# Optimization experiments

Hardware: AMD Instinct MI355X
Metric: run time of the kernel (lower is better)

Reference implementation:

```python
import jax, jax.numpy as jnp
import numpy as np

R = 2  # radius from sigma_wh == 1: int((1*6 - 1)/2) = 2 -> fixed 5x5 patch
P = 2 * R + 1

# Design matrix for log-domain Gaussian least-squares fit:
# log z = c0 + c1*x + c2*y + c3*x^2 + c4*y^2
_ys, _xs = np.meshgrid(np.arange(-R, R + 1), np.arange(-R, R + 1), indexing='ij')
_xs = _xs.reshape(-1).astype(np.float32)
_ys = _ys.reshape(-1).astype(np.float32)
_M = np.stack([np.ones_like(_xs), _xs, _ys, _xs ** 2, _ys ** 2], axis=1)  # [25,5]
PINV = jnp.asarray(np.linalg.pinv(_M))  # [5,25]


def _neg_loss(pred, gt):
    pos = (gt == 1.0).astype(pred.dtype)
    neg = (gt < 1.0).astype(pred.dtype)
    neg_w = (1.0 - gt) ** 4
    pos_loss = (jnp.log(pred) * (1.0 - pred) ** 2 * pos).sum()
    neg_loss = (jnp.log(1.0 - pred) * pred ** 2 * neg_w * neg).sum()
    num_pos = pos.sum()
    denom = jnp.where(num_pos == 0, 1.0, num_pos)
    return jnp.where(num_pos == 0, -neg_loss, -(pos_loss + neg_loss) / denom)


def setup_inputs() -> dict:
    key = jax.random.key(0)
    k1, k2, k3, k4 = jax.random.split(key, 4)
    B, C, H, W, O = 8, 80, 128, 128, 128
    return {
        'hm_out': jax.random.normal(k1, (B, C, H, W), jnp.float32),
        'hm_gt': jax.random.uniform(k2, (B, C, H, W), jnp.float32),
        'ct_ind': jax.random.randint(k3, (B, C, O, 2), 0, 124).astype(jnp.int32),
        'sigma_wh': jnp.ones((B, C, O, 2), jnp.float32),
        'hm_mask': jnp.ones((B, C, H, W), jnp.float32),
        'sigmawh_mask': jax.random.randint(k4, (B, C, O), 0, 2).astype(jnp.int32),
    }


def reference(hm_out, hm_gt, ct_ind, sigma_wh, hm_mask, sigmawh_mask):
    B, C, H, W = hm_out.shape
    O = ct_ind.shape[2]

    # --- focal loss (second call in original overwrites the first) ---
    hm_s = jax.nn.sigmoid(hm_out)
    pred = jnp.clip(hm_s, 1e-6, 1.0 - 1e-6)
    focal = _neg_loss(pred, hm_gt * hm_mask)

    # --- batched per-object 5x5 patch gather (replaces python triple loop) ---
    x = jnp.clip(ct_ind[..., 0], R, W - 1 - R)  # [B,C,O]
    y = jnp.clip(ct_ind[..., 1], R, H - 1 - R)
    off = jnp.arange(-R, R + 1)
    yy = y[..., None, None] + off[:, None]            # [B,C,O,P,1]
    xx = x[..., None, None] + off[None, :]            # [B,C,O,1,P]
    b_idx = jnp.arange(B)[:, None, None, None, None]
    c_idx = jnp.arange(C)[None, :, None, None, None]
    patch = hm_s[b_idx, c_idx, yy, xx]                # [B,C,O,P,P]
    logz = jnp.log(patch).reshape(B, C, O, P * P)

    # --- batched gaussian fit: least squares in log domain ---
    coef = jnp.einsum('bcop,kp->bcok', logz, PINV)    # [B,C,O,5]
    bx, by, ax, ay = coef[..., 1], coef[..., 2], coef[..., 3], coef[..., 4]
    ax_s = jnp.where(jnp.abs(ax) < 1e-12, -1.0, ax)
    ay_s = jnp.where(jnp.abs(ay) < 1e-12, -1.0, ay)
    sw2 = -0.5 / ax_s   # fitted variance along w
    sh2 = -0.5 / ay_s   # fitted variance along h
    mu_w = -bx / (2.0 * ax_s)
    mu_h = -by / (2.0 * ay_s)

    # original loop: obj in range(mask.sum()) and mask[obj]==1
    cnt = sigmawh_mask.sum(axis=-1)                                  # [B,C]
    in_loop = jnp.arange(O)[None, None, :] < cnt[..., None]
    valid = (sigmawh_mask == 1) & in_loop & (sw2 > 0) & (sh2 > 0)

    sgw = sigma_wh[..., 0]
    sgh = sigma_wh[..., 1]
    osw = jnp.where(valid, sw2, 1.0)
    osh = jnp.where(valid, sh2, 1.0)
    omw = jnp.where(valid, mu_w, 0.0)
    omh = jnp.where(valid, mu_h, 0.0)
    sgw2 = jnp.where(valid, sgw, 1.0) ** 2
    sgh2 = jnp.where(valid, sgh, 1.0) ** 2

    kl = (0.5 * jnp.log(sgw2 * sgh2 / (osw * osh)) - 1.0
          + 0.5 * (osw / sgw2 + osh / sgh2)
          + 0.5 * (omw ** 2 / sgw2 + omh ** 2 / sgh2))
    kl_sum = jnp.where(valid, kl, 0.0).sum()
    return (kl_sum, focal)
```

## Files before the change

### kernel.cpp

```cpp
#include <hip/hip_runtime.h>
#include <math.h>

#define Bn 8
#define Cn 80
#define Hn 128
#define Wn 128
#define On 128

#define FOCAL_BLOCKS 2560
#define FOCAL_THREADS 256
#define FOCAL_ITERS 4

#define WS_PL 0
#define WS_NL 2560
#define WS_NP 5120
#define WS_KL 7680
#define KL_BLOCKS (Bn * Cn)

#define LOG_EPS -13.815511f
#define LOG_1MEPS -1.0000005e-6f

__global__ __launch_bounds__(FOCAL_THREADS) void focal_kernel(
    const float4* __restrict__ hm_out, const float4* __restrict__ hm_gt,
    const float4* __restrict__ hm_mask, double* __restrict__ ws) {
    const int base = blockIdx.x * (FOCAL_THREADS * FOCAL_ITERS) + threadIdx.x;

    float4 xo[FOCAL_ITERS], xg[FOCAL_ITERS], xm[FOCAL_ITERS];
#pragma unroll
    for (int it = 0; it < FOCAL_ITERS; ++it) {
        int i = base + it * FOCAL_THREADS;
        xo[it] = hm_out[i];
        xg[it] = hm_gt[i];
        xm[it] = hm_mask[i];
    }

    float pl = 0.0f, nl = 0.0f, npos = 0.0f;
#pragma unroll
    for (int it = 0; it < FOCAL_ITERS; ++it) {
        const float* po = (const float*)&xo[it];
        const float* pg = (const float*)&xg[it];
        const float* pm = (const float*)&xm[it];
#pragma unroll
        for (int k = 0; k < 4; ++k) {
            float x = po[k];
            float g = pg[k] * pm[k];
            float e = expf(-x);
            float s = 1.0f / (1.0f + e);
            float ls = -logf(1.0f + e);
            float l1s = ls - x;
            float ls_c = fminf(fmaxf(ls, LOG_EPS), LOG_1MEPS);
            float l1s_c = fminf(fmaxf(l1s, LOG_EPS), LOG_1MEPS);
            float pred = fminf(fmaxf(s, 1e-6f), 1.0f - 1e-6f);

            float om = 1.0f - pred;
            float pos_c = ls_c * om * om;
            float omg = 1.0f - g;
            float w4 = omg * omg;
            w4 *= w4;
            float neg_c = l1s_c * pred * pred * w4;

            bool is_pos = (g == 1.0f);
            bool is_neg = (g < 1.0f);
            pl += is_pos ? pos_c : 0.0f;
            npos += is_pos ? 1.0f : 0.0f;
            nl += is_neg ? neg_c : 0.0f;
        }
    }

    for (int off = 32; off > 0; off >>= 1) {
        pl += __shfl_down(pl, off, 64);
        nl += __shfl_down(nl, off, 64);
        npos += __shfl_down(npos, off, 64);
    }
    __shared__ double sm[3 * (FOCAL_THREADS / 64)];
    int wave = threadIdx.x >> 6;
    int lane = threadIdx.x & 63;
    if (lane == 0) {
        sm[wave * 3 + 0] = (double)pl;
        sm[wave * 3 + 1] = (double)nl;
        sm[wave * 3 + 2] = (double)npos;
    }
    __syncthreads();
    if (threadIdx.x == 0) {
        double a = 0, b = 0, c = 0;
#pragma unroll
        for (int w = 0; w < FOCAL_THREADS / 64; ++w) {
            a += sm[w * 3 + 0];
            b += sm[w * 3 + 1];
            c += sm[w * 3 + 2];
        }
        ws[WS_PL + blockIdx.x] = a;
        ws[WS_NL + blockIdx.x] = b;
        ws[WS_NP + blockIdx.x] = c;
    }
}

__global__ __launch_bounds__(On) void kl_kernel(
    const float* __restrict__ hm_out, const int* __restrict__ ct_ind,
    const float* __restrict__ sigma_wh, const int* __restrict__ sigmawh_mask,
    double* __restrict__ ws) {
    int bc = blockIdx.x;
    int o = threadIdx.x;

    int m = sigmawh_mask[bc * On + o];

    __shared__ int smi[On];
    smi[o] = m;
    __syncthreads();
    for (int s = On / 2; s > 0; s >>= 1) {
        if (o < s) smi[o] += smi[o + s];
        __syncthreads();
    }
    int cnt = smi[0];

    float kl = 0.0f;
    if (m == 1 && o < cnt) {
        int xi = ct_ind[(bc * On + o) * 2 + 0];
        int yi = ct_ind[(bc * On + o) * 2 + 1];
        xi = min(max(xi, 2), Wn - 3);
        yi = min(max(yi, 2), Hn - 3);

        const float* base = hm_out + ((size_t)bc * Hn + yi) * Wn + xi;

        float v[25];
#pragma unroll
        for (int py = 0; py < 5; ++py)
#pragma unroll
            for (int px = 0; px < 5; ++px)
                v[py * 5 + px] = base[(py - 2) * Wn + (px - 2)];

        float Sbx = 0.f, Sby = 0.f, Sax = 0.f, Say = 0.f;
#pragma unroll
        for (int py = 0; py < 5; ++py) {
#pragma unroll
            for (int px = 0; px < 5; ++px) {
                float x = v[py * 5 + px];
                float lz = -logf(1.0f + expf(-x));
                float fx = (float)(px - 2), fy = (float)(py - 2);
                Sbx += fx * lz;
                Sby += fy * lz;
                Sax += (fx * fx - 2.0f) * lz;
                Say += (fy * fy - 2.0f) * lz;
            }
        }
        float bx = Sbx * (1.0f / 50.0f);
        float by = Sby * (1.0f / 50.0f);
        float ax = Sax * (1.0f / 70.0f);
        float ay = Say * (1.0f / 70.0f);

        float ax_s = (fabsf(ax) < 1e-12f) ? -1.0f : ax;
        float ay_s = (fabsf(ay) < 1e-12f) ? -1.0f : ay;
        float sw2 = -0.5f / ax_s;
        float sh2 = -0.5f / ay_s;

        if (sw2 > 0.0f && sh2 > 0.0f) {
            float mw = -bx / (2.0f * ax_s);
            float mh = -by / (2.0f * ay_s);
            float sgw = sigma_wh[(bc * On + o) * 2 + 0];
            float sgh = sigma_wh[(bc * On + o) * 2 + 1];
            float sgw2 = sgw * sgw;
            float sgh2 = sgh * sgh;
            kl = 0.5f * logf(sgw2 * sgh2 / (sw2 * sh2)) - 1.0f +
                 0.5f * (sw2 / sgw2 + sh2 / sgh2) +
                 0.5f * (mw * mw / sgw2 + mh * mh / sgh2);
        }
    }

    for (int off = 32; off > 0; off >>= 1) kl += __shfl_down(kl, off, 64);
    __shared__ double smd[On / 64];
    int wave = o >> 6;
    int lane = o & 63;
    if (lane == 0) smd[wave] = (double)kl;
    __syncthreads();
    if (o == 0) ws[WS_KL + bc] = smd[0] + smd[1];
}

__global__ __launch_bounds__(256) void finalize_kernel(
    const double* __restrict__ ws, float* __restrict__ out) {
    int t = threadIdx.x;
    double pl = 0, nl = 0, np = 0, kl = 0;
    for (int i = t; i < FOCAL_BLOCKS; i += 256) {
        pl += ws[WS_PL + i];
        nl += ws[WS_NL + i];
        np += ws[WS_NP + i];
    }
    for (int i = t; i < KL_BLOCKS; i += 256) kl += ws[WS_KL + i];

    __shared__ double sm[4 * 256];
    sm[t] = pl;
    sm[256 + t] = nl;
    sm[512 + t] = np;
    sm[768 + t] = kl;
    __syncthreads();
    for (int s = 128; s > 0; s >>= 1) {
        if (t < s) {
            sm[t] += sm[t + s];
            sm[256 + t] += sm[256 + t + s];
            sm[512 + t] += sm[512 + t + s];
            sm[768 + t] += sm[768 + t + s];
        }
        __syncthreads();
    }
    if (t == 0) {
        double focal = (sm[512] == 0.0) ? (-sm[256]) : (-(sm[0] + sm[256]) / sm[512]);
        out[0] = (float)sm[768];
        out[1] = (float)focal;
    }
}

extern "C" void kernel_launch(void* const* d_in, const int* in_sizes, int n_in,
                              void* d_out, int out_size, void* d_ws,
                              size_t ws_size, hipStream_t stream) {
    const float* hm_out       = (const float*)d_in[0];
    const float* hm_gt        = (const float*)d_in[1];
    const int*   ct_ind       = (const int*)d_in[2];
    const float* sigma_wh     = (const float*)d_in[3];
    const float* hm_mask      = (const float*)d_in[4];
    const int*   sigmawh_mask = (const int*)d_in[5];
    double* ws = (double*)d_ws;
    float* out = (float*)d_out;

    focal_kernel<<<FOCAL_BLOCKS, FOCAL_THREADS, 0, stream>>>(
        (const float4*)hm_out, (const float4*)hm_gt, (const float4*)hm_mask, ws);

    kl_kernel<<<KL_BLOCKS, On, 0, stream>>>(hm_out, ct_ind, sigma_wh,
                                            sigmawh_mask, ws);

    finalize_kernel<<<1, 256, 0, stream>>>(ws, out);
}
```

Baseline: 164.8 us.

## Fuse focal and KL kernels into one launch with lane-parallel patch fits

Merges the focal-loss and KL kernels into a single launch whose block ranges pick the role. The focal part now uses 2048 blocks with 5 float4 iterations each, and switches to fast __expf/__logf intrinsics. The KL part gives each object 32 lanes, one per pixel of its 5x5 patch, with shuffle reductions instead of one serial thread per object. The aim is to remove a launch boundary, let the KL work overlap the bandwidth-bound focal pass, and shorten the KL latency chain. The costs are slightly lower precision from the intrinsics and redundant mask-count reductions in every KL block.

```diff
diff --git a/kernel.cpp b/kernel.cpp
--- a/kernel.cpp
+++ b/kernel.cpp
@@ -7,203 +7,218 @@
 #define Wn 128
 #define On 128
 
-#define FOCAL_BLOCKS 2560
+#define FOCAL_BLOCKS 2048
 #define FOCAL_THREADS 256
-#define FOCAL_ITERS 4
+#define FOCAL_ITERS 5
+
+#define KL_BLOCKS (Bn * Cn * On / 8)
+#define TOTAL_BLOCKS (FOCAL_BLOCKS + KL_BLOCKS)
 
 #define WS_PL 0
-#define WS_NL 2560
-#define WS_NP 5120
-#define WS_KL 7680
-#define KL_BLOCKS (Bn * Cn)
+#define WS_NL FOCAL_BLOCKS
+#define WS_NP (2 * FOCAL_BLOCKS)
+#define WS_KL (3 * FOCAL_BLOCKS)
 
 #define LOG_EPS -13.815511f
 #define LOG_1MEPS -1.0000005e-6f
 
-__global__ __launch_bounds__(FOCAL_THREADS) void focal_kernel(
-    const float4* __restrict__ hm_out, const float4* __restrict__ hm_gt,
-    const float4* __restrict__ hm_mask, double* __restrict__ ws) {
-    const int base = blockIdx.x * (FOCAL_THREADS * FOCAL_ITERS) + threadIdx.x;
-
-    float4 xo[FOCAL_ITERS], xg[FOCAL_ITERS], xm[FOCAL_ITERS];
-#pragma unroll
-    for (int it = 0; it < FOCAL_ITERS; ++it) {
-        int i = base + it * FOCAL_THREADS;
-        xo[it] = hm_out[i];
-        xg[it] = hm_gt[i];
-        xm[it] = hm_mask[i];
-    }
-
-    float pl = 0.0f, nl = 0.0f, npos = 0.0f;
-#pragma unroll
-    for (int it = 0; it < FOCAL_ITERS; ++it) {
-        const float* po = (const float*)&xo[it];
-        const float* pg = (const float*)&xg[it];
-        const float* pm = (const float*)&xm[it];
-#pragma unroll
-        for (int k = 0; k < 4; ++k) {
-            float x = po[k];
-            float g = pg[k] * pm[k];
-            float e = expf(-x);
-            float s = 1.0f / (1.0f + e);
-            float ls = -logf(1.0f + e);
-            float l1s = ls - x;
-            float ls_c = fminf(fmaxf(ls, LOG_EPS), LOG_1MEPS);
-            float l1s_c = fminf(fmaxf(l1s, LOG_EPS), LOG_1MEPS);
-            float pred = fminf(fmaxf(s, 1e-6f), 1.0f - 1e-6f);
-
-            float om = 1.0f - pred;
-            float pos_c = ls_c * om * om;
-            float omg = 1.0f - g;
-            float w4 = omg * omg;
-            w4 *= w4;
-            float neg_c = l1s_c * pred * pred * w4;
-
-            bool is_pos = (g == 1.0f);
-            bool is_neg = (g < 1.0f);
-            pl += is_pos ? pos_c : 0.0f;
-            npos += is_pos ? 1.0f : 0.0f;
-            nl += is_neg ? neg_c : 0.0f;
-        }
-    }
+__global__ __launch_bounds__(256) void fused_kernel(
+    const float4* __restrict__ hm_out4, const float4* __restrict__ hm_gt4,
+    const float4* __restrict__ hm_mask4, const float* __restrict__ hm_out,
+    const int* __restrict__ ct_ind, const float* __restrict__ sigma_wh,
+    const int* __restrict__ sigmawh_mask, double* __restrict__ ws) {
+    __shared__ double sd[16];
+    __shared__ int si[128];
+
+    const int t = threadIdx.x;
+
+    if (blockIdx.x < FOCAL_BLOCKS) {
+        const int bid = blockIdx.x;
+        const int base = bid * (FOCAL_THREADS * FOCAL_ITERS) + t;
+
+        float4 xo[FOCAL_ITERS], xg[FOCAL_ITERS], xm[FOCAL_ITERS];
+#pragma unroll
+        for (int it = 0; it < FOCAL_ITERS; ++it)
+            xo[it] = hm_out4[base + it * FOCAL_THREADS];
+#pragma unroll
+        for (int it = 0; it < FOCAL_ITERS; ++it)
+            xg[it] = hm_gt4[base + it * FOCAL_THREADS];
+#pragma unroll
+        for (int it = 0; it < FOCAL_ITERS; ++it)
+            xm[it] = hm_mask4[base + it * FOCAL_THREADS];
+
+        float pl = 0.0f, nl = 0.0f, np = 0.0f;
+#pragma unroll
+        for (int it = 0; it < FOCAL_ITERS; ++it) {
+            const float* po = (const float*)&xo[it];
+            const float* pg = (const float*)&xg[it];
+            const float* pm = (const float*)&xm[it];
+#pragma unroll
+            for (int k = 0; k < 4; ++k) {
+                float x = po[k];
+                float g = pg[k] * pm[k];
+                float e = __expf(-x);
+                float s = 1.0f / (1.0f + e);
+                float ls = -__logf(1.0f + e);
+                float l1s = ls - x;
+                float ls_c = fminf(fmaxf(ls, LOG_EPS), LOG_1MEPS);
+                float l1s_c = fminf(fmaxf(l1s, LOG_EPS), LOG_1MEPS);
+                float pred = fminf(fmaxf(s, 1e-6f), 1.0f - 1e-6f);
+
+                float om = 1.0f - pred;
+                float pos_c = ls_c * om * om;
+                float omg = 1.0f - g;
+                float w4 = omg * omg;
+                w4 *= w4;
+                float neg_c = l1s_c * pred * pred * w4;
+
+                bool is_pos = (g == 1.0f);
+                bool is_neg = (g < 1.0f);
+                pl += is_pos ? pos_c : 0.0f;
+                np += is_pos ? 1.0f : 0.0f;
+                nl += is_neg ? neg_c : 0.0f;
+            }
+        }
+
+        for (int off = 32; off > 0; off >>= 1) {
+            pl += __shfl_down(pl, off, 64);
+            nl += __shfl_down(nl, off, 64);
+            np += __shfl_down(np, off, 64);
+        }
+        int wave = t >> 6, lane = t & 63;
+        if (lane == 0) {
+            sd[wave * 3 + 0] = (double)pl;
+            sd[wave * 3 + 1] = (double)nl;
+            sd[wave * 3 + 2] = (double)np;
+        }
+        __syncthreads();
+        if (t == 0) {
+            double a = 0, b = 0, c = 0;
+#pragma unroll
+            for (int w = 0; w < 4; ++w) {
+                a += sd[w * 3 + 0];
+                b += sd[w * 3 + 1];
+                c += sd[w * 3 + 2];
+            }
+            ws[WS_PL + bid] = a;
+            ws[WS_NL + bid] = b;
+            ws[WS_NP + bid] = c;
+        }
+    } else {
+        const int kb = blockIdx.x - FOCAL_BLOCKS;
+        const int bc = kb >> 4;
+        const int o_base = (kb & 15) * 8;
+
+        if (t < 128) si[t] = sigmawh_mask[bc * On + t];
+        __syncthreads();
+
+        const int w = t >> 6, lane = t & 63;
+        const int half = lane >> 5, pix = lane & 31;
+        const int o = o_base + w * 2 + half;
+        const int m = si[o];
+        __syncthreads();
+        for (int s = 64; s > 0; s >>= 1) {
+            if (t < s) si[t] += si[t + s];
+            __syncthreads();
+        }
+        const int cnt = si[0];
+
+        float kl = 0.0f;
+        if (m == 1 && o < cnt) {
+            int gi = (bc * On + o) * 2;
+            int xi = min(max(ct_ind[gi + 0], 2), Wn - 3);
+            int yi = min(max(ct_ind[gi + 1], 2), Hn - 3);
+
+            float Sbx = 0.f, Sby = 0.f, Sax = 0.f, Say = 0.f;
+            if (pix < 25) {
+                int py = pix / 5;
+                int px = pix - py * 5;
+                float v = hm_out[((size_t)bc * Hn + (yi + py - 2)) * Wn +
+                                 (xi + px - 2)];
+                float lz = -__logf(1.0f + __expf(-v));
+                float fx = (float)(px - 2), fy = (float)(py - 2);
+                Sbx = fx * lz;
+                Sby = fy * lz;
+                Sax = (fx * fx - 2.0f) * lz;
+                Say = (fy * fy - 2.0f) * lz;
+            }
+#pragma unroll
+            for (int off = 16; off > 0; off >>= 1) {
+                Sbx += __shfl_xor(Sbx, off, 64);
+                Sby += __shfl_xor(Sby, off, 64);
+                Sax += __shfl_xor(Sax, off, 64);
+                Say += __shfl_xor(Say, off, 64);
+            }
+            float bx = Sbx * (1.0f / 50.0f);
+            float by = Sby * (1.0f / 50.0f);
+            float ax = Sax * (1.0f / 70.0f);
+            float ay = Say * (1.0f / 70.0f);
+
+            float ax_s = (fabsf(ax) < 1e-12f) ? -1.0f : ax;
+            float ay_s = (fabsf(ay) < 1e-12f) ? -1.0f : ay;
+            float sw2 = -0.5f / ax_s;
+            float sh2 = -0.5f / ay_s;
+
+            if (sw2 > 0.0f && sh2 > 0.0f) {
+                float mw = -bx / (2.0f * ax_s);
+                float mh = -by / (2.0f * ay_s);
+                float sgw = sigma_wh[gi + 0];
+                float sgh = sigma_wh[gi + 1];
+                float sgw2 = sgw * sgw;
+                float sgh2 = sgh * sgh;
+                kl = 0.5f * __logf(sgw2 * sgh2 / (sw2 * sh2)) - 1.0f +
+                     0.5f * (sw2 / sgw2 + sh2 / sgh2) +
+                     0.5f * (mw * mw / sgw2 + mh * mh / sgh2);
+            }
+        }
+        if (pix == 0) sd[w * 2 + half] = (double)kl;
+        __syncthreads();
+        if (t == 0) {
+            double s = 0;
+#pragma unroll
+            for (int i = 0; i < 8; ++i) s += sd[i];
+            ws[WS_KL + kb] = s;
+        }
+    }
+}
+
+__global__ __launch_bounds__(1024) void finalize_kernel(
+    const double* __restrict__ ws, float* __restrict__ out) {
+    int t = threadIdx.x;
+    double pl = 0, nl = 0, np = 0, kl = 0;
+    for (int i = t; i < FOCAL_BLOCKS; i += 1024) {
+        pl += ws[WS_PL + i];
+        nl += ws[WS_NL + i];
+        np += ws[WS_NP + i];
+    }
+    for (int i = t; i < KL_BLOCKS; i += 1024) kl += ws[WS_KL + i];
 
     for (int off = 32; off > 0; off >>= 1) {
         pl += __shfl_down(pl, off, 64);
         nl += __shfl_down(nl, off, 64);
-        npos += __shfl_down(npos, off, 64);
-    }
-    __shared__ double sm[3 * (FOCAL_THREADS / 64)];
-    int wave = threadIdx.x >> 6;
-    int lane = threadIdx.x & 63;
+        np += __shfl_down(np, off, 64);
+        kl += __shfl_down(kl, off, 64);
+    }
+    __shared__ double sm[16 * 4];
+    int wave = t >> 6, lane = t & 63;
     if (lane == 0) {
-        sm[wave * 3 + 0] = (double)pl;
-        sm[wave * 3 + 1] = (double)nl;
-        sm[wave * 3 + 2] = (double)npos;
+        sm[wave * 4 + 0] = pl;
+        sm[wave * 4 + 1] = nl;
+        sm[wave * 4 + 2] = np;
+        sm[wave * 4 + 3] = kl;
     }
     __syncthreads();
-    if (threadIdx.x == 0) {
-        double a = 0, b = 0, c = 0;
-#pragma unroll
-        for (int w = 0; w < FOCAL_THREADS / 64; ++w) {
-            a += sm[w * 3 + 0];
-            b += sm[w * 3 + 1];
-            c += sm[w * 3 + 2];
-        }
-        ws[WS_PL + blockIdx.x] = a;
-        ws[WS_NL + blockIdx.x] = b;
-        ws[WS_NP + blockIdx.x] = c;
-    }
-}
-
-__global__ __launch_bounds__(On) void kl_kernel(
-    const float* __restrict__ hm_out, const int* __restrict__ ct_ind,
-    const float* __restrict__ sigma_wh, const int* __restrict__ sigmawh_mask,
-    double* __restrict__ ws) {
-    int bc = blockIdx.x;
-    int o = threadIdx.x;
-
-    int m = sigmawh_mask[bc * On + o];
-
-    __shared__ int smi[On];
-    smi[o] = m;
-    __syncthreads();
-    for (int s = On / 2; s > 0; s >>= 1) {
-        if (o < s) smi[o] += smi[o + s];
-        __syncthreads();
-    }
-    int cnt = smi[0];
-
-    float kl = 0.0f;
-    if (m == 1 && o < cnt) {
-        int xi = ct_ind[(bc * On + o) * 2 + 0];
-        int yi = ct_ind[(bc * On + o) * 2 + 1];
-        xi = min(max(xi, 2), Wn - 3);
-        yi = min(max(yi, 2), Hn - 3);
-
-        const float* base = hm_out + ((size_t)bc * Hn + yi) * Wn + xi;
-
-        float v[25];
-#pragma unroll
-        for (int py = 0; py < 5; ++py)
-#pragma unroll
-            for (int px = 0; px < 5; ++px)
-                v[py * 5 + px] = base[(py - 2) * Wn + (px - 2)];
-
-        float Sbx = 0.f, Sby = 0.f, Sax = 0.f, Say = 0.f;
-#pragma unroll
-        for (int py = 0; py < 5; ++py) {
-#pragma unroll
-            for (int px = 0; px < 5; ++px) {
-                float x = v[py * 5 + px];
-                float lz = -logf(1.0f + expf(-x));
-                float fx = (float)(px - 2), fy = (float)(py - 2);
-                Sbx += fx * lz;
-                Sby += fy * lz;
-                Sax += (fx * fx - 2.0f) * lz;
-                Say += (fy * fy - 2.0f) * lz;
-            }
-        }
-        float bx = Sbx * (1.0f / 50.0f);
-        float by = Sby * (1.0f / 50.0f);
-        float ax = Sax * (1.0f / 70.0f);
-        float ay = Say * (1.0f / 70.0f);
-
-        float ax_s = (fabsf(ax) < 1e-12f) ? -1.0f : ax;
-        float ay_s = (fabsf(ay) < 1e-12f) ? -1.0f : ay;
-        float sw2 = -0.5f / ax_s;
-        float sh2 = -0.5f / ay_s;
-
-        if (sw2 > 0.0f && sh2 > 0.0f) {
-            float mw = -bx / (2.0f * ax_s);
-            float mh = -by / (2.0f * ay_s);
-            float sgw = sigma_wh[(bc * On + o) * 2 + 0];
-            float sgh = sigma_wh[(bc * On + o) * 2 + 1];
-            float sgw2 = sgw * sgw;
-            float sgh2 = sgh * sgh;
-            kl = 0.5f * logf(sgw2 * sgh2 / (sw2 * sh2)) - 1.0f +
-                 0.5f * (sw2 / sgw2 + sh2 / sgh2) +
-                 0.5f * (mw * mw / sgw2 + mh * mh / sgh2);
-        }
-    }
-
-    for (int off = 32; off > 0; off >>= 1) kl += __shfl_down(kl, off, 64);
-    __shared__ double smd[On / 64];
-    int wave = o >> 6;
-    int lane = o & 63;
-    if (lane == 0) smd[wave] = (double)kl;
-    __syncthreads();
-    if (o == 0) ws[WS_KL + bc] = smd[0] + smd[1];
-}
-
-__global__ __launch_bounds__(256) void finalize_kernel(
-    const double* __restrict__ ws, float* __restrict__ out) {
-    int t = threadIdx.x;
-    double pl = 0, nl = 0, np = 0, kl = 0;
-    for (int i = t; i < FOCAL_BLOCKS; i += 256) {
-        pl += ws[WS_PL + i];
-        nl += ws[WS_NL + i];
-        np += ws[WS_NP + i];
-    }
-    for (int i = t; i < KL_BLOCKS; i += 256) kl += ws[WS_KL + i];
-
-    __shared__ double sm[4 * 256];
-    sm[t] = pl;
-    sm[256 + t] = nl;
-    sm[512 + t] = np;
-    sm[768 + t] = kl;
-    __syncthreads();
-    for (int s = 128; s > 0; s >>= 1) {
-        if (t < s) {
-            sm[t] += sm[t + s];
-            sm[256 + t] += sm[256 + t + s];
-            sm[512 + t] += sm[512 + t + s];
-            sm[768 + t] += sm[768 + t + s];
-        }
-        __syncthreads();
-    }
     if (t == 0) {
-        double focal = (sm[512] == 0.0) ? (-sm[256]) : (-(sm[0] + sm[256]) / sm[512]);
-        out[0] = (float)sm[768];
+        double a = 0, b = 0, c = 0, d = 0;
+#pragma unroll
+        for (int w = 0; w < 16; ++w) {
+            a += sm[w * 4 + 0];
+            b += sm[w * 4 + 1];
+            c += sm[w * 4 + 2];
+            d += sm[w * 4 + 3];
+        }
+        double focal = (c == 0.0) ? (-b) : (-(a + b) / c);
+        out[0] = (float)d;
         out[1] = (float)focal;
     }
 }
@@ -220,11 +235,9 @@
     double* ws = (double*)d_ws;
     float* out = (float*)d_out;
 
-    focal_kernel<<<FOCAL_BLOCKS, FOCAL_THREADS, 0, stream>>>(
-        (const float4*)hm_out, (const float4*)hm_gt, (const float4*)hm_mask, ws);
-
-    kl_kernel<<<KL_BLOCKS, On, 0, stream>>>(hm_out, ct_ind, sigma_wh,
-                                            sigmawh_mask, ws);
-
-    finalize_kernel<<<1, 256, 0, stream>>>(ws, out);
+    fused_kernel<<<TOTAL_BLOCKS, 256, 0, stream>>>(
+        (const float4*)hm_out, (const float4*)hm_gt, (const float4*)hm_mask,
+        hm_out, ct_ind, sigma_wh, sigmawh_mask, ws);
+
+    finalize_kernel<<<1, 1024, 0, stream>>>(ws, out);
 }
```

Measured after the change: 167.6 us. Within noise of the previous version (+1.7%).
